# Performance work log

Measured on AMD Instinct MI355X. Metric: run time of the kernel, lower is better.

The kernel has to match this reference:

```python
import jax, jax.numpy as jnp
import numpy as np

N_NODES = 100000
N_EDGES = 1600000
IN_DIM = 64
HIDDEN = 128
N_CLASSES = 16


def setup_inputs() -> dict:
    key = jax.random.key(0)
    ks = jax.random.split(key, 16)
    inp = {
        'feats': jax.random.normal(ks[0], (N_NODES, IN_DIM), dtype=jnp.float32),
        'H1_src': jax.random.randint(ks[1], (N_EDGES,), 0, N_NODES),
        'H1_dst': jax.random.randint(ks[2], (N_EDGES,), 0, N_NODES),
        'H2_src': jax.random.randint(ks[3], (N_EDGES,), 0, N_NODES),
        'H2_dst': jax.random.randint(ks[4], (N_EDGES,), 0, N_NODES),
        'W1_self1': 0.1 * jax.random.normal(ks[5], (IN_DIM, HIDDEN), dtype=jnp.float32),
        'W1_neigh1': 0.1 * jax.random.normal(ks[6], (IN_DIM, HIDDEN), dtype=jnp.float32),
        'W1_self2': 0.1 * jax.random.normal(ks[7], (HIDDEN, HIDDEN), dtype=jnp.float32),
        'W1_neigh2': 0.1 * jax.random.normal(ks[8], (HIDDEN, HIDDEN), dtype=jnp.float32),
        'W1_lin': 0.1 * jax.random.normal(ks[9], (HIDDEN, N_CLASSES), dtype=jnp.float32),
        'W2_self1': 0.1 * jax.random.normal(ks[10], (IN_DIM, HIDDEN), dtype=jnp.float32),
        'W2_neigh1': 0.1 * jax.random.normal(ks[11], (IN_DIM, HIDDEN), dtype=jnp.float32),
        'W2_self2': 0.1 * jax.random.normal(ks[12], (HIDDEN, HIDDEN), dtype=jnp.float32),
        'W2_neigh2': 0.1 * jax.random.normal(ks[13], (HIDDEN, HIDDEN), dtype=jnp.float32),
        'W2_lin': 0.1 * jax.random.normal(ks[14], (HIDDEN, N_CLASSES), dtype=jnp.float32),
    }
    return inp


def _neighbor_mean(x, src, dst, n_nodes):
    # gather messages along edges, sum into destinations, divide by in-degree
    msg = x[src]                                        # [E, d] irregular gather
    agg = jax.ops.segment_sum(msg, dst, num_segments=n_nodes)  # [N, d]
    deg = jax.ops.segment_sum(jnp.ones((src.shape[0],), x.dtype), dst,
                              num_segments=n_nodes)     # [N]
    return agg / jnp.maximum(deg, 1.0)[:, None]         # zero-degree nodes -> 0


def _sage_layer(x, src, dst, W_self, W_neigh):
    h_neigh = _neighbor_mean(x, src, dst, x.shape[0])
    return jax.nn.relu(x @ W_self + h_neigh @ W_neigh)


def _graphsage(src, dst, x, Ws1, Wn1, Ws2, Wn2, Wlin):
    h = _sage_layer(x, src, dst, Ws1, Wn1)
    h = _sage_layer(h, src, dst, Ws2, Wn2)
    graph_rep = jnp.mean(h, axis=0)                     # dgl.mean_nodes (single graph)
    return jax.nn.sigmoid(graph_rep @ Wlin)             # [num_classes]


def reference(feats, H1_src, H1_dst, H2_src, H2_dst,
              W1_self1, W1_neigh1, W1_self2, W1_neigh2, W1_lin,
              W2_self1, W2_neigh1, W2_self2, W2_neigh2, W2_lin):
    rep1 = _graphsage(H1_src, H1_dst, feats, W1_self1, W1_neigh1, W1_self2, W1_neigh2, W1_lin)
    rep2 = _graphsage(H2_src, H2_dst, feats, W2_self1, W2_neigh1, W2_self2, W2_neigh2, W2_lin)
    return (rep1 + rep2) / 2.0
```

## Files before the change

### kernel.cpp

```cpp
#include <hip/hip_runtime.h>
#include <hip/hip_fp16.h>

#define NN 100000
#define NE 1600000
#define IND 64
#define HID 128
#define NCLS 16
#define GEMMB (NN / 16)
#define RBLK 50
#define NCRS 98
#define CAPC 18432
#define CAPF 352
#define NDCAP 48
#define EPB1 8192
#define NBG1 ((NE + EPB1 - 1) / EPB1)
#define FCH 8192

typedef float v2f __attribute__((ext_vector_type(2)));
typedef __attribute__((ext_vector_type(8))) short short8v;
typedef __attribute__((ext_vector_type(4))) float f32x4;

__device__ __forceinline__ float fp8_sw_unpack(unsigned b) {
    unsigned s = (b >> 7) & 1u, em = b & 0x7fu;
    return __uint_as_float((s << 31) | (em << 20)) * 0x1p+120f;
}
__device__ __forceinline__ unsigned fp8_sw_pack(float f) {
    float c = fminf(fmaxf(f, -448.f), 448.f) * 0x1p-120f;
    unsigned b = __float_as_uint(c);
    unsigned s = b >> 31; b &= 0x7fffffffu;
    b = b + 0x7ffffu + ((b >> 20) & 1u);
    unsigned em = b >> 20;
    if (em > 0x7eu) em = 0x7eu;
    return (s << 7) | em;
}
template<bool HI>
__device__ __forceinline__ unsigned pk8(float a, float b, unsigned old) {
#if __has_builtin(__builtin_amdgcn_cvt_pk_fp8_f32)
    return (unsigned)__builtin_amdgcn_cvt_pk_fp8_f32(a, b, (int)old, HI);
#else
    unsigned v = fp8_sw_pack(a) | (fp8_sw_pack(b) << 8);
    return HI ? ((old & 0x0000ffffu) | (v << 16)) : ((old & 0xffff0000u) | v);
#endif
}
template<bool HI>
__device__ __forceinline__ v2f upk8(unsigned u) {
#if __has_builtin(__builtin_amdgcn_cvt_pk_f32_fp8)
    return __builtin_amdgcn_cvt_pk_f32_fp8((int)u, HI);
#else
    unsigned x = HI ? (u >> 16) : u;
    v2f r; r.x = fp8_sw_unpack(x & 0xffu); r.y = fp8_sw_unpack((x >> 8) & 0xffu);
    return r;
#endif
}

__device__ __forceinline__ short f2bf(float f) {
    unsigned u = __float_as_uint(f);
    return (short)((u + 0x7fffu + ((u >> 16) & 1u)) >> 16);
}

__device__ __forceinline__ void bacc8v(v2f* a, uint4 v) {
    a[0] += upk8<false>(v.x); a[1] += upk8<true>(v.x);
    a[2] += upk8<false>(v.y); a[3] += upk8<true>(v.y);
    a[4] += upk8<false>(v.z); a[5] += upk8<true>(v.z);
    a[6] += upk8<false>(v.w); a[7] += upk8<true>(v.w);
}

__device__ __forceinline__ short8v mk8(const v2f* a, float iv) {
    short8v r;
    r[0] = f2bf(a[0].x * iv); r[1] = f2bf(a[0].y * iv);
    r[2] = f2bf(a[1].x * iv); r[3] = f2bf(a[1].y * iv);
    r[4] = f2bf(a[2].x * iv); r[5] = f2bf(a[2].y * iv);
    r[6] = f2bf(a[3].x * iv); r[7] = f2bf(a[3].y * iv);
    return r;
}

__global__ void conv16_kernel(const float4* __restrict__ x, uint4* __restrict__ o, int n16) {
    int i = blockIdx.x * blockDim.x + threadIdx.x;
    if (i >= n16) return;
    float4 v0 = x[4 * i + 0], v1 = x[4 * i + 1], v2 = x[4 * i + 2], v3 = x[4 * i + 3];
    uint4 u;
    u.x = pk8<true>(v0.z, v0.w, pk8<false>(v0.x, v0.y, 0u));
    u.y = pk8<true>(v1.z, v1.w, pk8<false>(v1.x, v1.y, 0u));
    u.z = pk8<true>(v2.z, v2.w, pk8<false>(v2.x, v2.y, 0u));
    u.w = pk8<true>(v3.z, v3.w, pk8<false>(v3.x, v3.y, 0u));
    o[i] = u;
}

__global__ void packW_all(const float* __restrict__ Ws1a, const float* __restrict__ Wn1a,
                          const float* __restrict__ Ws1b, const float* __restrict__ Wn1b,
                          const float* __restrict__ Ws2a, const float* __restrict__ Wn2a,
                          const float* __restrict__ Ws2b, const float* __restrict__ Wn2b,
                          short* __restrict__ out) {
    int t = blockIdx.x * 256 + threadIdx.x;
    if (t >= 12288) return;
    const float *Ws, *Wn; short* o; int KS;
    if (t < 2048)      { Ws = Ws1a; Wn = Wn1a; o = out;         KS = 64;  }
    else if (t < 4096) { Ws = Ws1b; Wn = Wn1b; o = out + 16384; KS = 64;  t -= 2048; }
    else if (t < 8192) { Ws = Ws2a; Wn = Wn2a; o = out + 32768; KS = 128; t -= 4096; }
    else               { Ws = Ws2b; Wn = Wn2b; o = out + 65536; KS = 128; t -= 8192; }
    int l = t & 63, f = t >> 6, nn = f & 7, kk = f >> 3;
    int col = nn * 16 + (l & 15);
    int k0 = kk * 32 + ((l >> 4) * 8);
    unsigned short v[8];
#pragma unroll
    for (int j = 0; j < 8; j++) {
        int k = k0 + j;
        float x = (k < KS) ? Ws[k * 128 + col] : Wn[(k - KS) * 128 + col];
        v[j] = (unsigned short)f2bf(x);
    }
    uint4 u;
    u.x = (unsigned)v[0] | ((unsigned)v[1] << 16);
    u.y = (unsigned)v[2] | ((unsigned)v[3] << 16);
    u.z = (unsigned)v[4] | ((unsigned)v[5] << 16);
    u.w = (unsigned)v[6] | ((unsigned)v[7] << 16);
    ((uint4*)o)[t] = u;
}

__global__ __launch_bounds__(512) void place_coarse(
    const int* __restrict__ s0, const int* __restrict__ d0,
    const int* __restrict__ s1, const int* __restrict__ d1,
    int* __restrict__ gcurC,
    unsigned* __restrict__ pc0, unsigned* __restrict__ pc1) {
    __shared__ unsigned ebuf[EPB1];
    __shared__ int h[128], off[128];
    __shared__ int hb[NCRS];
    const int bi = blockIdx.x;
    const int g = bi >= NBG1;
    const int* src = g ? s1 : s0;
    const int* dst = g ? d1 : d0;
    unsigned* pc = g ? pc1 : pc0;
    const int base = (g ? bi - NBG1 : bi) * EPB1;
    const int tid = threadIdx.x;
    int nle = NE - base; if (nle > EPB1) nle = EPB1;

    if (tid < 128) h[tid] = 0;
    __syncthreads();
    for (int j = tid; j < nle; j += 512) atomicAdd(&h[dst[base + j] >> 10], 1);
    __syncthreads();
    if (tid < 128) off[tid] = h[tid];
    __syncthreads();
    for (int o = 1; o < 128; o <<= 1) {
        int v = (tid < 128 && tid >= o) ? off[tid - o] : 0;
        __syncthreads();
        if (tid < 128) off[tid] += v;
        __syncthreads();
    }
    if (tid < NCRS) hb[tid] = h[tid] ? atomicAdd(&gcurC[g * NCRS + tid], h[tid]) : 0;
    __syncthreads();
    if (tid < 128) h[tid] = off[tid] - h[tid];
    __syncthreads();
    for (int j = tid; j < nle; j += 512) {
        int d = dst[base + j];
        int b = d >> 10;
        int pos = atomicAdd(&h[b], 1);
        ebuf[pos] = (unsigned)src[base + j] | ((unsigned)(d & 1023) << 17);
    }
    __syncthreads();
    const int wv = tid >> 6, lane = tid & 63;
    for (int b = wv; b < NCRS; b += 8) {
        int beg = b ? off[b - 1] : 0;
        int run = off[b] - beg;
        int gb = hb[b];
        if (gb + run > CAPC) run = CAPC - gb;
        for (int i = lane; i < run; i += 64)
            pc[(size_t)b * CAPC + gb + i] = ebuf[beg + i];
    }
}

__global__ __launch_bounds__(512) void place_fine(
    const unsigned* __restrict__ pc0, const unsigned* __restrict__ pc1,
    const int* __restrict__ gcurC,
    unsigned* __restrict__ pf0, unsigned* __restrict__ pf1,
    int* __restrict__ fcnt0, int* __restrict__ fcnt1) {
    __shared__ unsigned obuf[FCH];
    __shared__ int h2[64], off2[64], cur2[64], gcur2[64];
    const int bi = blockIdx.x;
    const int g = bi >= NCRS;
    const int c = g ? bi - NCRS : bi;
    const unsigned* pc = g ? pc1 : pc0;
    unsigned* pf = g ? pf1 : pf0;
    int* fcnt = g ? fcnt1 : fcnt0;
    int ecnt = gcurC[g * NCRS + c];
    if (ecnt > CAPC) ecnt = CAPC;
    const size_t cb = (size_t)c * CAPC;
    const int tid = threadIdx.x;
    const int wv = tid >> 6, lane = tid & 63;

    if (tid < 64) gcur2[tid] = 0;
    __syncthreads();
    for (int s = 0; s < ecnt; s += FCH) {
        int n = ecnt - s; if (n > FCH) n = FCH;
        if (tid < 64) h2[tid] = 0;
        __syncthreads();
        for (int e = tid; e < n; e += 512)
            atomicAdd(&h2[(pc[cb + s + e] >> 21) & 63], 1);
        __syncthreads();
        if (tid < 64) off2[tid] = h2[tid];
        __syncthreads();
        for (int o = 1; o < 64; o <<= 1) {
            int v = (tid < 64 && tid >= o) ? off2[tid - o] : 0;
            __syncthreads();
            if (tid < 64) off2[tid] += v;
            __syncthreads();
        }
        if (tid < 64) cur2[tid] = off2[tid] - h2[tid];
        __syncthreads();
        for (int e = tid; e < n; e += 512) {
            unsigned u = pc[cb + s + e];
            int sub = (u >> 21) & 63;
            int pos = atomicAdd(&cur2[sub], 1);
            obuf[pos] = (u & 0x1FFFFu) | (((u >> 17) & 15u) << 17);
        }
        __syncthreads();
        for (int sub = wv; sub < 64; sub += 8) {
            int beg = sub ? off2[sub - 1] : 0;
            int run = off2[sub] - beg;
            int gb = gcur2[sub];
            if (gb + run > CAPF) run = CAPF - gb;
            for (int i = lane; i < run; i += 64)
                pf[(size_t)(c * 64 + sub) * CAPF + gb + i] = obuf[beg + i];
        }
        __syncthreads();
        if (tid < 64) gcur2[tid] += h2[tid];
        __syncthreads();
    }
    if (tid < 64) {
        int v = gcur2[tid];
        fcnt[c * 64 + tid] = v > CAPF ? CAPF : v;
    }
}

template<int KS, bool REDUCE>
__global__ __launch_bounds__(256) void sage_fused(
    const float* __restrict__ xin,
    const unsigned* __restrict__ x8a, const unsigned* __restrict__ x8b,
    const unsigned* __restrict__ pf0, const unsigned* __restrict__ pf1,
    const int* __restrict__ fcnt0, const int* __restrict__ fcnt1,
    const short* __restrict__ Wfa, const short* __restrict__ Wfb,
    float* __restrict__ outRa, float* __restrict__ outRb,
    unsigned* __restrict__ outHa, unsigned* __restrict__ outHb) {
    constexpr int KT = (2 * KS) / 32;
    __shared__ short8v sA[KT * 64];
    __shared__ float otile[REDUCE ? 1 : 16 * 132];
    __shared__ int lcnt[16];
    __shared__ int ssrcL[16 * NDCAP];

    const int tid = threadIdx.x;
    const int g = blockIdx.x >= GEMMB;
    const int gid = g ? blockIdx.x - GEMMB : blockIdx.x;
    const int n0 = gid * 16;
    const unsigned* x8 = g ? x8b : x8a;
    const unsigned* pf = g ? pf1 : pf0;
    const int* fcnt = g ? fcnt1 : fcnt0;
    const short8v* Wf = (const short8v*)(g ? Wfb : Wfa);
    const uint4* xb4 = (const uint4*)x8;

    if (tid < 16) lcnt[tid] = 0;
    __syncthreads();

    {
        int ecnt = fcnt[gid];
        for (int e = tid; e < ecnt; e += 256) {
            unsigned u = pf[(size_t)gid * CAPF + e];
            int loc = (u >> 17) & 15;
            int pos = atomicAdd(&lcnt[loc], 1);
            if (pos < NDCAP) ssrcL[loc * NDCAP + pos] = (int)(u & 0x1FFFFu);
        }
    }

    if (tid < 128) {
        if constexpr (KS == IND) {
            int node = tid >> 3, r = tid & 7;
            float4 v0 = ((const float4*)xin)[(size_t)(n0 + node) * 16 + r * 2];
            float4 v1 = ((const float4*)xin)[(size_t)(n0 + node) * 16 + r * 2 + 1];
            short8v s;
            s[0] = f2bf(v0.x); s[1] = f2bf(v0.y); s[2] = f2bf(v0.z); s[3] = f2bf(v0.w);
            s[4] = f2bf(v1.x); s[5] = f2bf(v1.y); s[6] = f2bf(v1.z); s[7] = f2bf(v1.w);
            int kk = r >> 2, kg = r & 3;
            sA[(kk * 64 + kg * 16 + node) ^ (kk & 7)] = s;
        } else {
            int node = tid >> 3, c8 = tid & 7;
            uint4 u = xb4[(size_t)(n0 + node) * 8 + c8];
            v2f a[8];
            a[0] = upk8<false>(u.x); a[1] = upk8<true>(u.x);
            a[2] = upk8<false>(u.y); a[3] = upk8<true>(u.y);
            a[4] = upk8<false>(u.z); a[5] = upk8<true>(u.z);
            a[6] = upk8<false>(u.w); a[7] = upk8<true>(u.w);
            int kk = c8 >> 1, kg0 = (c8 & 1) * 2;
            sA[(kk * 64 + kg0 * 16 + node) ^ (kk & 7)]       = mk8(a, 1.0f);
            sA[(kk * 64 + (kg0 + 1) * 16 + node) ^ (kk & 7)] = mk8(a + 4, 1.0f);
        }
    }
    __syncthreads();

    {
        const int nb = tid >> 4;
        const int degt = lcnt[nb];
        const int degc = degt > NDCAP ? NDCAP : degt;
        const int* L = &ssrcL[nb * NDCAP];
        v2f a[8];
#pragma unroll
        for (int j = 0; j < 8; j++) a[j] = (v2f)(0.0f);

        if constexpr (KS == HID) {
            const int l = tid & 7;
            const int h = (tid >> 3) & 1;
            int i = h;
            for (; i + 2 < degc; i += 4) {
                int i0 = L[i], i1 = L[i + 2];
                uint4 v0 = xb4[(size_t)i0 * 8 + l];
                uint4 v1 = xb4[(size_t)i1 * 8 + l];
                bacc8v(a, v0);
                bacc8v(a, v1);
            }
            if (i < degc) bacc8v(a, xb4[(size_t)L[i] * 8 + l]);
#pragma unroll
            for (int j = 0; j < 8; j++) {
                a[j].x += __shfl_xor(a[j].x, 8);
                a[j].y += __shfl_xor(a[j].y, 8);
            }
            if (h == 0) {
                float iv = 1.0f / fmaxf((float)degt, 1.0f);
                int kk = 4 + (l >> 1), kg0 = (l & 1) * 2;
                sA[(kk * 64 + kg0 * 16 + nb) ^ (kk & 7)]       = mk8(a, iv);
                sA[(kk * 64 + (kg0 + 1) * 16 + nb) ^ (kk & 7)] = mk8(a + 4, iv);
            }
        } else {
            const int sub = tid & 15;
            const int l = sub & 3;
            const int h = sub >> 2;
            int i = h;
            for (; i + 4 < degc; i += 8) {
                int i0 = L[i], i1 = L[i + 4];
                uint4 v0 = xb4[(size_t)i0 * 4 + l];
                uint4 v1 = xb4[(size_t)i1 * 4 + l];
                bacc8v(a, v0);
                bacc8v(a, v1);
            }
            if (i < degc) bacc8v(a, xb4[(size_t)L[i] * 4 + l]);
#pragma unroll
            for (int j = 0; j < 8; j++) {
                a[j].x += __shfl_xor(a[j].x, 4);
                a[j].y += __shfl_xor(a[j].y, 4);
            }
#pragma unroll
            for (int j = 0; j < 8; j++) {
                a[j].x += __shfl_xor(a[j].x, 8);
                a[j].y += __shfl_xor(a[j].y, 8);
            }
            if (h == 0) {
                float iv = 1.0f / fmaxf((float)degt, 1.0f);
                int kk = 2 + (l >> 1), kg0 = (l & 1) * 2;
                sA[(kk * 64 + kg0 * 16 + nb) ^ (kk & 7)]       = mk8(a, iv);
                sA[(kk * 64 + (kg0 + 1) * 16 + nb) ^ (kk & 7)] = mk8(a + 4, iv);
            }
        }
    }
    __syncthreads();

    const int lane = tid & 63;
    const int q = tid >> 6;
    const int r15 = lane & 15;
    const int kg = lane >> 4;
    f32x4 acc0 = {0.f, 0.f, 0.f, 0.f};
    f32x4 acc1 = {0.f, 0.f, 0.f, 0.f};

#pragma unroll
    for (int kk = 0; kk < KT; kk++) {
        short8v af = sA[(kk * 64 + lane) ^ (kk & 7)];
        short8v b0 = Wf[(kk * 8 + 2 * q + 0) * 64 + lane];
        short8v b1 = Wf[(kk * 8 + 2 * q + 1) * 64 + lane];
        acc0 = __builtin_amdgcn_mfma_f32_16x16x32_bf16(af, b0, acc0, 0, 0, 0);
        acc1 = __builtin_amdgcn_mfma_f32_16x16x32_bf16(af, b1, acc1, 0, 0, 0);
    }

    if constexpr (!REDUCE) {
#pragma unroll
        for (int i = 0; i < 4; i++) {
            otile[(kg * 4 + i) * 132 + 32 * q + r15]      = fmaxf(acc0[i], 0.f);
            otile[(kg * 4 + i) * 132 + 32 * q + 16 + r15] = fmaxf(acc1[i], 0.f);
        }
        __syncthreads();
        int node = tid >> 4, c = tid & 15;
        float4 x0 = *(const float4*)&otile[node * 132 + c * 8];
        float4 x1 = *(const float4*)&otile[node * 132 + c * 8 + 4];
        unsigned w0 = pk8<false>(x0.x, x0.y, 0u); w0 = pk8<true>(x0.z, x0.w, w0);
        unsigned w1 = pk8<false>(x1.x, x1.y, 0u); w1 = pk8<true>(x1.z, x1.w, w1);
        uint2* o8 = (uint2*)(g ? outHb : outHa);
        o8[(size_t)(n0 + node) * 16 + c] = make_uint2(w0, w1);
    } else {
        float s0 = 0.f, s1 = 0.f;
#pragma unroll
        for (int i = 0; i < 4; i++) {
            s0 += fmaxf(acc0[i], 0.f);
            s1 += fmaxf(acc1[i], 0.f);
        }
        s0 += __shfl_xor(s0, 16); s0 += __shfl_xor(s0, 32);
        s1 += __shfl_xor(s1, 16); s1 += __shfl_xor(s1, 32);
        float* outR = g ? outRb : outRa;
        size_t base = (size_t)gid * 128;
        if (lane < 16)      outR[base + 32 * q + lane] = s0;
        else if (lane < 32) outR[base + 32 * q + 16 + (lane & 15)] = s1;
    }
}

__global__ void reduce1_kernel(const float* __restrict__ p0, const float* __restrict__ p1,
                               float* __restrict__ p2) {
    const int bb = blockIdx.x;
    const int tid = threadIdx.x;
    const int g = tid >> 7;
    const int col = tid & 127;
    const float* p = g ? p1 : p0;
    const int per = GEMMB / RBLK;
    float s = 0.0f;
    for (int r = 0; r < per; r++) s += p[(size_t)(bb * per + r) * 128 + col];
    p2[(size_t)bb * 256 + tid] = s;
}

__global__ void final_kernel(const float* __restrict__ p2,
                             const float* __restrict__ Wlin1,
                             const float* __restrict__ Wlin2,
                             float* __restrict__ out) {
    __shared__ float rep[2][HID];
    __shared__ float sg[32];
    const int tid = threadIdx.x;
    float s = 0.0f;
    for (int r = 0; r < RBLK; r++) s += p2[r * 256 + tid];
    rep[tid >> 7][tid & 127] = s * (1.0f / (float)NN);
    __syncthreads();
    if (tid < 32) {
        const int g = tid / 16;
        const int c = tid % 16;
        const float* W = g ? Wlin2 : Wlin1;
        float a = 0.0f;
        for (int k = 0; k < HID; k++) a += rep[g][k] * W[k * NCLS + c];
        sg[tid] = 1.0f / (1.0f + expf(-a));
    }
    __syncthreads();
    if (tid < 16) out[tid] = 0.5f * (sg[tid] + sg[16 + tid]);
}

extern "C" void kernel_launch(void* const* d_in, const int* in_sizes, int n_in,
                              void* d_out, int out_size, void* d_ws, size_t ws_size,
                              hipStream_t stream) {
    const float* feats = (const float*)d_in[0];
    const int* srcp[2] = {(const int*)d_in[1], (const int*)d_in[3]};
    const int* dstp[2] = {(const int*)d_in[2], (const int*)d_in[4]};
    const float* Ws1[2] = {(const float*)d_in[5], (const float*)d_in[10]};
    const float* Wn1[2] = {(const float*)d_in[6], (const float*)d_in[11]};
    const float* Ws2[2] = {(const float*)d_in[7], (const float*)d_in[12]};
    const float* Wn2[2] = {(const float*)d_in[8], (const float*)d_in[13]};
    const float* Wlin[2] = {(const float*)d_in[9], (const float*)d_in[14]};

    char* w = (char*)d_ws;
    unsigned* fb8 = (unsigned*)w;   w += (size_t)NN * IND;
    unsigned* h18a = (unsigned*)w;  w += (size_t)NN * HID;
    unsigned* h18b = (unsigned*)w;  w += (size_t)NN * HID;
    unsigned* pf0 = (unsigned*)w;   w += (size_t)GEMMB * CAPF * 4;
    unsigned* pf1 = (unsigned*)w;   w += (size_t)GEMMB * CAPF * 4;
    float* part0 = (float*)w;       w += (size_t)GEMMB * 128 * 4;
    float* part1 = (float*)w;       w += (size_t)GEMMB * 128 * 4;
    float* p2 = (float*)w;          w += (size_t)RBLK * 256 * 4;
    int* fcnt0 = (int*)w;           w += (size_t)NCRS * 64 * 4;
    int* fcnt1 = (int*)w;           w += (size_t)NCRS * 64 * 4;
    int* gcurC = (int*)w;           w += 2 * NCRS * 4;
    w = (char*)(((uintptr_t)w + 15) & ~(uintptr_t)15);
    short* wpk = (short*)w;         w += 98304 * 2;
    unsigned* pc0 = h18a;
    unsigned* pc1 = h18b;

    conv16_kernel<<<(NN * IND / 16 + 255) / 256, 256, 0, stream>>>(
        (const float4*)feats, (uint4*)fb8, NN * IND / 16);

    packW_all<<<48, 256, 0, stream>>>(Ws1[0], Wn1[0], Ws1[1], Wn1[1],
                                      Ws2[0], Wn2[0], Ws2[1], Wn2[1], wpk);

    (void)hipMemsetAsync(gcurC, 0, 2 * NCRS * 4, stream);
    place_coarse<<<2 * NBG1, 512, 0, stream>>>(srcp[0], dstp[0], srcp[1], dstp[1],
                                               gcurC, pc0, pc1);
    place_fine<<<2 * NCRS, 512, 0, stream>>>(pc0, pc1, gcurC, pf0, pf1, fcnt0, fcnt1);

    sage_fused<IND, false><<<2 * GEMMB, 256, 0, stream>>>(
        feats, fb8, fb8, pf0, pf1, fcnt0, fcnt1,
        wpk, wpk + 16384,
        nullptr, nullptr, h18a, h18b);

    sage_fused<HID, true><<<2 * GEMMB, 256, 0, stream>>>(
        nullptr, h18a, h18b, pf0, pf1, fcnt0, fcnt1,
        wpk + 32768, wpk + 65536,
        part0, part1, nullptr, nullptr);

    reduce1_kernel<<<RBLK, 256, 0, stream>>>(part0, part1, p2);
    final_kernel<<<1, 256, 0, stream>>>(p2, Wlin[0], Wlin[1], (float*)d_out);
}
```

Measured before the change: 306.0 us.

## Split fine bucketing across more blocks and double threads per sage block

```diff
diff --git a/kernel.cpp b/kernel.cpp
--- a/kernel.cpp
+++ b/kernel.cpp
@@ -14,7 +14,8 @@
 #define NDCAP 48
 #define EPB1 8192
 #define NBG1 ((NE + EPB1 - 1) / EPB1)
-#define FCH 8192
+#define FSPLIT 4
+#define FSPAN ((CAPC + FSPLIT - 1) / FSPLIT)
 
 typedef float v2f __attribute__((ext_vector_type(2)));
 typedef __attribute__((ext_vector_type(8))) short short8v;
@@ -171,71 +172,68 @@
     const unsigned* __restrict__ pc0, const unsigned* __restrict__ pc1,
     const int* __restrict__ gcurC,
     unsigned* __restrict__ pf0, unsigned* __restrict__ pf1,
-    int* __restrict__ fcnt0, int* __restrict__ fcnt1) {
-    __shared__ unsigned obuf[FCH];
-    __shared__ int h2[64], off2[64], cur2[64], gcur2[64];
+    int* __restrict__ fcur) {
+    __shared__ unsigned obuf[FSPAN];
+    __shared__ int h2[64], off2[64], cur2[64], gb2[64];
     const int bi = blockIdx.x;
-    const int g = bi >= NCRS;
-    const int c = g ? bi - NCRS : bi;
+    const int g = bi >= NCRS * FSPLIT;
+    const int idx = g ? bi - NCRS * FSPLIT : bi;
+    const int c = idx >> 2, part = idx & (FSPLIT - 1);
     const unsigned* pc = g ? pc1 : pc0;
     unsigned* pf = g ? pf1 : pf0;
-    int* fcnt = g ? fcnt1 : fcnt0;
+    int* fc = fcur + (size_t)g * NCRS * 64;
     int ecnt = gcurC[g * NCRS + c];
     if (ecnt > CAPC) ecnt = CAPC;
-    const size_t cb = (size_t)c * CAPC;
+    int span = (ecnt + FSPLIT - 1) / FSPLIT;
+    int st = part * span;
+    int en = st + span; if (en > ecnt) en = ecnt;
+    int n = en - st; if (n < 0) n = 0;
+    const size_t cb = (size_t)c * CAPC + st;
     const int tid = threadIdx.x;
     const int wv = tid >> 6, lane = tid & 63;
 
-    if (tid < 64) gcur2[tid] = 0;
-    __syncthreads();
-    for (int s = 0; s < ecnt; s += FCH) {
-        int n = ecnt - s; if (n > FCH) n = FCH;
-        if (tid < 64) h2[tid] = 0;
+    if (tid < 64) h2[tid] = 0;
+    __syncthreads();
+    for (int e = tid; e < n; e += 512)
+        atomicAdd(&h2[(pc[cb + e] >> 21) & 63], 1);
+    __syncthreads();
+    if (tid < 64) {
+        gb2[tid] = h2[tid] ? atomicAdd(&fc[c * 64 + tid], h2[tid]) : 0;
+        off2[tid] = h2[tid];
+    }
+    __syncthreads();
+    for (int o = 1; o < 64; o <<= 1) {
+        int v = (tid < 64 && tid >= o) ? off2[tid - o] : 0;
         __syncthreads();
-        for (int e = tid; e < n; e += 512)
-            atomicAdd(&h2[(pc[cb + s + e] >> 21) & 63], 1);
+        if (tid < 64) off2[tid] += v;
         __syncthreads();
-        if (tid < 64) off2[tid] = h2[tid];
-        __syncthreads();
-        for (int o = 1; o < 64; o <<= 1) {
-            int v = (tid < 64 && tid >= o) ? off2[tid - o] : 0;
-            __syncthreads();
-            if (tid < 64) off2[tid] += v;
-            __syncthreads();
-        }
-        if (tid < 64) cur2[tid] = off2[tid] - h2[tid];
-        __syncthreads();
-        for (int e = tid; e < n; e += 512) {
-            unsigned u = pc[cb + s + e];
-            int sub = (u >> 21) & 63;
-            int pos = atomicAdd(&cur2[sub], 1);
-            obuf[pos] = (u & 0x1FFFFu) | (((u >> 17) & 15u) << 17);
-        }
-        __syncthreads();
-        for (int sub = wv; sub < 64; sub += 8) {
-            int beg = sub ? off2[sub - 1] : 0;
-            int run = off2[sub] - beg;
-            int gb = gcur2[sub];
-            if (gb + run > CAPF) run = CAPF - gb;
-            for (int i = lane; i < run; i += 64)
-                pf[(size_t)(c * 64 + sub) * CAPF + gb + i] = obuf[beg + i];
-        }
-        __syncthreads();
-        if (tid < 64) gcur2[tid] += h2[tid];
-        __syncthreads();
-    }
-    if (tid < 64) {
-        int v = gcur2[tid];
-        fcnt[c * 64 + tid] = v > CAPF ? CAPF : v;
+    }
+    if (tid < 64) cur2[tid] = off2[tid] - h2[tid];
+    __syncthreads();
+    for (int e = tid; e < n; e += 512) {
+        unsigned u = pc[cb + e];
+        int sub = (u >> 21) & 63;
+        int pos = atomicAdd(&cur2[sub], 1);
+        obuf[pos] = (u & 0x1FFFFu) | (((u >> 17) & 15u) << 17);
+    }
+    __syncthreads();
+    for (int sub = wv; sub < 64; sub += 8) {
+        int beg = sub ? off2[sub - 1] : 0;
+        int run = off2[sub] - beg;
+        int gb = gb2[sub];
+        if (gb >= CAPF) run = 0;
+        else if (gb + run > CAPF) run = CAPF - gb;
+        for (int i = lane; i < run; i += 64)
+            pf[(size_t)(c * 64 + sub) * CAPF + gb + i] = obuf[beg + i];
     }
 }
 
 template<int KS, bool REDUCE>
-__global__ __launch_bounds__(256) void sage_fused(
+__global__ __launch_bounds__(512) void sage_fused(
     const float* __restrict__ xin,
     const unsigned* __restrict__ x8a, const unsigned* __restrict__ x8b,
     const unsigned* __restrict__ pf0, const unsigned* __restrict__ pf1,
-    const int* __restrict__ fcnt0, const int* __restrict__ fcnt1,
+    const int* __restrict__ fcur,
     const short* __restrict__ Wfa, const short* __restrict__ Wfb,
     float* __restrict__ outRa, float* __restrict__ outRb,
     unsigned* __restrict__ outHa, unsigned* __restrict__ outHb) {
@@ -251,7 +249,7 @@
     const int n0 = gid * 16;
     const unsigned* x8 = g ? x8b : x8a;
     const unsigned* pf = g ? pf1 : pf0;
-    const int* fcnt = g ? fcnt1 : fcnt0;
+    const int* fc = fcur + (size_t)g * NCRS * 64;
     const short8v* Wf = (const short8v*)(g ? Wfb : Wfa);
     const uint4* xb4 = (const uint4*)x8;
 
@@ -259,8 +257,9 @@
     __syncthreads();
 
     {
-        int ecnt = fcnt[gid];
-        for (int e = tid; e < ecnt; e += 256) {
+        int ecnt = fc[gid];
+        if (ecnt > CAPF) ecnt = CAPF;
+        for (int e = tid; e < ecnt; e += 512) {
             unsigned u = pf[(size_t)gid * CAPF + e];
             int loc = (u >> 17) & 15;
             int pos = atomicAdd(&lcnt[loc], 1);
@@ -294,7 +293,8 @@
     __syncthreads();
 
     {
-        const int nb = tid >> 4;
+        const int nb = tid >> 5;
+        const int sub = tid & 31;
         const int degt = lcnt[nb];
         const int degc = degt > NDCAP ? NDCAP : degt;
         const int* L = &ssrcL[nb * NDCAP];
@@ -303,11 +303,11 @@
         for (int j = 0; j < 8; j++) a[j] = (v2f)(0.0f);
 
         if constexpr (KS == HID) {
-            const int l = tid & 7;
-            const int h = (tid >> 3) & 1;
+            const int l = sub & 7;
+            const int h = sub >> 3;
             int i = h;
-            for (; i + 2 < degc; i += 4) {
-                int i0 = L[i], i1 = L[i + 2];
+            for (; i + 4 < degc; i += 8) {
+                int i0 = L[i], i1 = L[i + 4];
                 uint4 v0 = xb4[(size_t)i0 * 8 + l];
                 uint4 v1 = xb4[(size_t)i1 * 8 + l];
                 bacc8v(a, v0);
@@ -316,8 +316,8 @@
             if (i < degc) bacc8v(a, xb4[(size_t)L[i] * 8 + l]);
 #pragma unroll
             for (int j = 0; j < 8; j++) {
-                a[j].x += __shfl_xor(a[j].x, 8);
-                a[j].y += __shfl_xor(a[j].y, 8);
+                a[j].x += __shfl_xor(a[j].x, 8);  a[j].y += __shfl_xor(a[j].y, 8);
+                a[j].x += __shfl_xor(a[j].x, 16); a[j].y += __shfl_xor(a[j].y, 16);
             }
             if (h == 0) {
                 float iv = 1.0f / fmaxf((float)degt, 1.0f);
@@ -326,12 +326,11 @@
                 sA[(kk * 64 + (kg0 + 1) * 16 + nb) ^ (kk & 7)] = mk8(a + 4, iv);
             }
         } else {
-            const int sub = tid & 15;
             const int l = sub & 3;
             const int h = sub >> 2;
             int i = h;
-            for (; i + 4 < degc; i += 8) {
-                int i0 = L[i], i1 = L[i + 4];
+            for (; i + 8 < degc; i += 16) {
+                int i0 = L[i], i1 = L[i + 8];
                 uint4 v0 = xb4[(size_t)i0 * 4 + l];
                 uint4 v1 = xb4[(size_t)i1 * 4 + l];
                 bacc8v(a, v0);
@@ -340,13 +339,9 @@
             if (i < degc) bacc8v(a, xb4[(size_t)L[i] * 4 + l]);
 #pragma unroll
             for (int j = 0; j < 8; j++) {
-                a[j].x += __shfl_xor(a[j].x, 4);
-                a[j].y += __shfl_xor(a[j].y, 4);
-            }
-#pragma unroll
-            for (int j = 0; j < 8; j++) {
-                a[j].x += __shfl_xor(a[j].x, 8);
-                a[j].y += __shfl_xor(a[j].y, 8);
+                a[j].x += __shfl_xor(a[j].x, 4);  a[j].y += __shfl_xor(a[j].y, 4);
+                a[j].x += __shfl_xor(a[j].x, 8);  a[j].y += __shfl_xor(a[j].y, 8);
+                a[j].x += __shfl_xor(a[j].x, 16); a[j].y += __shfl_xor(a[j].y, 16);
             }
             if (h == 0) {
                 float iv = 1.0f / fmaxf((float)degt, 1.0f);
@@ -362,45 +357,36 @@
     const int q = tid >> 6;
     const int r15 = lane & 15;
     const int kg = lane >> 4;
-    f32x4 acc0 = {0.f, 0.f, 0.f, 0.f};
-    f32x4 acc1 = {0.f, 0.f, 0.f, 0.f};
+    f32x4 acc = {0.f, 0.f, 0.f, 0.f};
 
 #pragma unroll
     for (int kk = 0; kk < KT; kk++) {
         short8v af = sA[(kk * 64 + lane) ^ (kk & 7)];
-        short8v b0 = Wf[(kk * 8 + 2 * q + 0) * 64 + lane];
-        short8v b1 = Wf[(kk * 8 + 2 * q + 1) * 64 + lane];
-        acc0 = __builtin_amdgcn_mfma_f32_16x16x32_bf16(af, b0, acc0, 0, 0, 0);
-        acc1 = __builtin_amdgcn_mfma_f32_16x16x32_bf16(af, b1, acc1, 0, 0, 0);
+        short8v b0 = Wf[(kk * 8 + q) * 64 + lane];
+        acc = __builtin_amdgcn_mfma_f32_16x16x32_bf16(af, b0, acc, 0, 0, 0);
     }
 
     if constexpr (!REDUCE) {
 #pragma unroll
-        for (int i = 0; i < 4; i++) {
-            otile[(kg * 4 + i) * 132 + 32 * q + r15]      = fmaxf(acc0[i], 0.f);
-            otile[(kg * 4 + i) * 132 + 32 * q + 16 + r15] = fmaxf(acc1[i], 0.f);
+        for (int i = 0; i < 4; i++)
+            otile[(kg * 4 + i) * 132 + 16 * q + r15] = fmaxf(acc[i], 0.f);
+        __syncthreads();
+        if (tid < 256) {
+            int node = tid >> 4, c = tid & 15;
+            float4 x0 = *(const float4*)&otile[node * 132 + c * 8];
+            float4 x1 = *(const float4*)&otile[node * 132 + c * 8 + 4];
+            unsigned w0 = pk8<false>(x0.x, x0.y, 0u); w0 = pk8<true>(x0.z, x0.w, w0);
+            unsigned w1 = pk8<false>(x1.x, x1.y, 0u); w1 = pk8<true>(x1.z, x1.w, w1);
+            uint2* o8 = (uint2*)(g ? outHb : outHa);
+            o8[(size_t)(n0 + node) * 16 + c] = make_uint2(w0, w1);
         }
-        __syncthreads();
-        int node = tid >> 4, c = tid & 15;
-        float4 x0 = *(const float4*)&otile[node * 132 + c * 8];
-        float4 x1 = *(const float4*)&otile[node * 132 + c * 8 + 4];
-        unsigned w0 = pk8<false>(x0.x, x0.y, 0u); w0 = pk8<true>(x0.z, x0.w, w0);
-        unsigned w1 = pk8<false>(x1.x, x1.y, 0u); w1 = pk8<true>(x1.z, x1.w, w1);
-        uint2* o8 = (uint2*)(g ? outHb : outHa);
-        o8[(size_t)(n0 + node) * 16 + c] = make_uint2(w0, w1);
     } else {
-        float s0 = 0.f, s1 = 0.f;
-#pragma unroll
-        for (int i = 0; i < 4; i++) {
-            s0 += fmaxf(acc0[i], 0.f);
-            s1 += fmaxf(acc1[i], 0.f);
-        }
+        float s0 = 0.f;
+#pragma unroll
+        for (int i = 0; i < 4; i++) s0 += fmaxf(acc[i], 0.f);
         s0 += __shfl_xor(s0, 16); s0 += __shfl_xor(s0, 32);
-        s1 += __shfl_xor(s1, 16); s1 += __shfl_xor(s1, 32);
         float* outR = g ? outRb : outRa;
-        size_t base = (size_t)gid * 128;
-        if (lane < 16)      outR[base + 32 * q + lane] = s0;
-        else if (lane < 32) outR[base + 32 * q + 16 + (lane & 15)] = s1;
+        if (lane < 16) outR[(size_t)gid * 128 + 16 * q + lane] = s0;
     }
 }
 
@@ -461,8 +447,7 @@
     float* part0 = (float*)w;       w += (size_t)GEMMB * 128 * 4;
     float* part1 = (float*)w;       w += (size_t)GEMMB * 128 * 4;
     float* p2 = (float*)w;          w += (size_t)RBLK * 256 * 4;
-    int* fcnt0 = (int*)w;           w += (size_t)NCRS * 64 * 4;
-    int* fcnt1 = (int*)w;           w += (size_t)NCRS * 64 * 4;
+    int* fcur = (int*)w;            w += (size_t)2 * NCRS * 64 * 4;
     int* gcurC = (int*)w;           w += 2 * NCRS * 4;
     w = (char*)(((uintptr_t)w + 15) & ~(uintptr_t)15);
     short* wpk = (short*)w;         w += 98304 * 2;
@@ -476,17 +461,18 @@
                                       Ws2[0], Wn2[0], Ws2[1], Wn2[1], wpk);
 
     (void)hipMemsetAsync(gcurC, 0, 2 * NCRS * 4, stream);
+    (void)hipMemsetAsync(fcur, 0, (size_t)2 * NCRS * 64 * 4, stream);
     place_coarse<<<2 * NBG1, 512, 0, stream>>>(srcp[0], dstp[0], srcp[1], dstp[1],
                                                gcurC, pc0, pc1);
-    place_fine<<<2 * NCRS, 512, 0, stream>>>(pc0, pc1, gcurC, pf0, pf1, fcnt0, fcnt1);
-
-    sage_fused<IND, false><<<2 * GEMMB, 256, 0, stream>>>(
-        feats, fb8, fb8, pf0, pf1, fcnt0, fcnt1,
+    place_fine<<<2 * NCRS * FSPLIT, 512, 0, stream>>>(pc0, pc1, gcurC, pf0, pf1, fcur);
+
+    sage_fused<IND, false><<<2 * GEMMB, 512, 0, stream>>>(
+        feats, fb8, fb8, pf0, pf1, fcur,
         wpk, wpk + 16384,
         nullptr, nullptr, h18a, h18b);
 
-    sage_fused<HID, true><<<2 * GEMMB, 256, 0, stream>>>(
-        nullptr, h18a, h18b, pf0, pf1, fcnt0, fcnt1,
+    sage_fused<HID, true><<<2 * GEMMB, 512, 0, stream>>>(
+        nullptr, h18a, h18b, pf0, pf1, fcur,
         wpk + 32768, wpk + 65536,
         part0, part1, nullptr, nullptr);
 
```

Result: slower. 336.6 us (+10.0%).
